# Kernel optimization log

Measured on AMD Instinct MI355X. Metric: run time of the kernel, lower is better.

Reference implementation:

```python
import jax, jax.numpy as jnp
import numpy as np
import math

HIDDEN = 1024
HEADS = 16
HEAD_DIM = HIDDEN // HEADS
B, S = 2, 2048


def setup_inputs() -> dict:
    key = jax.random.key(0)
    ks = jax.random.split(key, 10)
    std = 1.0 / math.sqrt(HIDDEN)
    mk = lambda k: (jax.random.normal(k, (HIDDEN, HIDDEN), jnp.float32) * std)
    return {
        "hidden_states": jax.random.normal(ks[0], (B, S, HIDDEN), jnp.float32),
        "attention_mask": jnp.zeros((B, 1, 1, S), jnp.float32),
        "wq": mk(ks[1]), "bq": jnp.zeros((HIDDEN,), jnp.float32),
        "wk": mk(ks[2]), "bk": jnp.zeros((HIDDEN,), jnp.float32),
        "wv": mk(ks[3]), "bv": jnp.zeros((HIDDEN,), jnp.float32),
        "wo": mk(ks[4]), "bo": jnp.zeros((HIDDEN,), jnp.float32),
    }


def reference(hidden_states, attention_mask, wq, bq, wk, bk, wv, bv, wo, bo):
    b, s, _ = hidden_states.shape
    scale = math.sqrt(HEAD_DIM)
    # projections (torch Linear: x @ W.T + b); weights stored as [out, in]
    q = hidden_states @ wq.T + bq
    k = hidden_states @ wk.T + bk
    v = hidden_states @ wv.T + bv
    # [B, H, S, D]
    q = q.reshape(b, s, HEADS, HEAD_DIM).transpose(0, 2, 1, 3)
    k = k.reshape(b, s, HEADS, HEAD_DIM).transpose(0, 2, 1, 3)
    v = v.reshape(b, s, HEADS, HEAD_DIM).transpose(0, 2, 1, 3)
    scores = jnp.einsum("bhqd,bhkd->bhqk", q, k) / scale
    scores = scores + attention_mask  # broadcast [B,1,1,S]
    weights = jax.nn.softmax(scores, axis=-1)  # dropout = identity (eval)
    out = jnp.einsum("bhqk,bhkd->bhqd", weights, v)
    out = out.transpose(0, 2, 1, 3).reshape(b, s, HIDDEN)
    out = out @ wo.T + bo
    return out
```

## Files before the change

### kernel.cpp

```cpp
#include <hip/hip_runtime.h>
#include <hip/hip_bf16.h>

typedef __bf16 bf16_t;
typedef __bf16 bf16x8 __attribute__((ext_vector_type(8)));
typedef _Float16 f16x4 __attribute__((ext_vector_type(4)));
typedef _Float16 f16x8 __attribute__((ext_vector_type(8)));
typedef float f32x4 __attribute__((ext_vector_type(4)));

#define SEQ    2048
#define NH     16
#define HD     64
#define HIDDEN 1024
#define LOG2E  1.44269504f

#if __has_builtin(__builtin_amdgcn_exp2f)
#define EXP2F(x) __builtin_amdgcn_exp2f(x)
#else
#define EXP2F(x) exp2f(x)
#endif

__device__ __forceinline__ bf16_t to_bf16(float f) { return (bf16_t)f; }

__device__ __forceinline__ void async16(const void* g, void* l) {
    __builtin_amdgcn_global_load_lds((const __attribute__((address_space(1))) void*)g,
                                     (__attribute__((address_space(3))) void*)l, 16, 0, 0);
}

__global__ __launch_bounds__(256) void cvt_kernel(
    const float* __restrict__ s0, bf16_t* __restrict__ d0, int c0,
    const float* __restrict__ s1, bf16_t* __restrict__ d1, int c1,
    const float* __restrict__ s2, bf16_t* __restrict__ d2, int c2,
    const float* __restrict__ s3, bf16_t* __restrict__ d3, int c3,
    const float* __restrict__ s4, bf16_t* __restrict__ d4, int c4,
    const float* __restrict__ s5, float* __restrict__ d5)
{
    int blk = blockIdx.x;
    const float* s; bf16_t* d;
    if (blk < c0)              { s = s0; d = d0; }
    else if ((blk -= c0) < c1) { s = s1; d = d1; }
    else if ((blk -= c1) < c2) { s = s2; d = d2; }
    else if ((blk -= c2) < c3) { s = s3; d = d3; }
    else if ((blk -= c3) < c4) { s = s4; d = d4; }
    else {
        blk -= c4;
        const size_t base = (size_t)blk * 2048 + threadIdx.x * 8;
        float4 a = *(const float4*)&s5[base];
        float4 b = *(const float4*)&s5[base + 4];
        a.x *= LOG2E; a.y *= LOG2E; a.z *= LOG2E; a.w *= LOG2E;
        b.x *= LOG2E; b.y *= LOG2E; b.z *= LOG2E; b.w *= LOG2E;
        *(float4*)&d5[base] = a;
        *(float4*)&d5[base + 4] = b;
        return;
    }
    const size_t base = (size_t)blk * 2048 + threadIdx.x * 8;
    const float4 a = *(const float4*)&s[base];
    const float4 b = *(const float4*)&s[base + 4];
    bf16x8 o;
    o[0] = (bf16_t)a.x; o[1] = (bf16_t)a.y; o[2] = (bf16_t)a.z; o[3] = (bf16_t)a.w;
    o[4] = (bf16_t)b.x; o[5] = (bf16_t)b.y; o[6] = (bf16_t)b.z; o[7] = (bf16_t)b.w;
    *(bf16x8*)&d[base] = o;
}

__global__ __launch_bounds__(256, 3) void qkv_kernel(
    const bf16_t* __restrict__ X,
    const bf16_t* __restrict__ wq, const bf16_t* __restrict__ wk, const bf16_t* __restrict__ wv,
    const float* __restrict__ bq, const float* __restrict__ bk, const float* __restrict__ bv,
    bf16_t* __restrict__ qws, bf16_t* __restrict__ kws, _Float16* __restrict__ vws)
{
    __shared__ __align__(16) bf16_t Sh[16384];
    const int z = blockIdx.z;
    const bf16_t* Wsel = (z == 0) ? wq : (z == 1) ? wk : wv;
    const float*  bsel = (z == 0) ? bq : (z == 1) ? bk : bv;
    const int m0 = blockIdx.y * 128, n0 = blockIdx.x * 128;

    const int t = threadIdx.x, lane = t & 63, w = t >> 6;
    const int w0 = w & 1, w1 = w >> 1, l15 = lane & 15, q4 = lane >> 4;

    f32x4 acc[4][4];
#pragma unroll
    for (int i = 0; i < 4; i++)
#pragma unroll
        for (int j = 0; j < 4; j++) acc[i][j] = f32x4{0.f, 0.f, 0.f, 0.f};

    auto stage = [&](int kt, int buf) {
#pragma unroll
        for (int j = 0; j < 2; j++) {
            const int s = j * 256 + t;
            const int row = s >> 2, c = (s & 3) ^ (row & 3);
            const int lb = buf * 8192 + (j * 256 + w * 64) * 8;
            async16(&X[(size_t)(m0 + row) * HIDDEN + kt + c * 8], &Sh[lb]);
            async16(&Wsel[(size_t)(n0 + row) * HIDDEN + kt + c * 8], &Sh[lb + 4096]);
        }
    };
    stage(0, 0);

    for (int it = 0; it < 32; it++) {
        const int cur = it & 1;
        __syncthreads();
        if (it < 31) stage((it + 1) * 32, cur ^ 1);
        const bf16_t* As = &Sh[cur * 8192];
        const bf16_t* Bs = &Sh[cur * 8192 + 4096];
        bf16x8 af[4];
#pragma unroll
        for (int ti = 0; ti < 4; ti++) {
            const int ra = w0 * 64 + ti * 16 + l15;
            af[ti] = *(const bf16x8*)&As[ra * 32 + (q4 ^ (ra & 3)) * 8];
        }
#pragma unroll
        for (int tj = 0; tj < 4; tj++) {
            const int rb = w1 * 64 + tj * 16 + l15;
            const bf16x8 bfr = *(const bf16x8*)&Bs[rb * 32 + (q4 ^ (rb & 3)) * 8];
#pragma unroll
            for (int ti = 0; ti < 4; ti++)
                acc[ti][tj] = __builtin_amdgcn_mfma_f32_16x16x32_bf16(af[ti], bfr, acc[ti][tj], 0, 0, 0);
        }
    }
    __syncthreads();

    if (z < 2) {
#pragma unroll
        for (int tj = 0; tj < 4; tj++) {
            const int n = w1 * 64 + tj * 16 + l15;
            const float bb = bsel[n0 + n];
            const int ch = (n >> 3), sub = n & 7;
#pragma unroll
            for (int ti = 0; ti < 4; ti++)
#pragma unroll
                for (int r = 0; r < 4; r++) {
                    const int m = w0 * 64 + ti * 16 + q4 * 4 + r;
                    Sh[m * 128 + ((ch ^ (m & 15)) << 3) + sub] = to_bf16(acc[ti][tj][r] + bb);
                }
        }
        __syncthreads();
        bf16_t* dst = (z == 0) ? qws : kws;
#pragma unroll
        for (int i = 0; i < 8; i++) {
            const int g = i * 256 + t;
            const int row = g >> 4, c = g & 15;
            const bf16x8 vv = *(const bf16x8*)&Sh[row * 128 + ((c ^ (row & 15)) << 3)];
            *(bf16x8*)&dst[(size_t)(m0 + row) * HIDDEN + n0 + c * 8] = vv;
        }
    } else {
        _Float16* Vt = (_Float16*)Sh;
#pragma unroll
        for (int tj = 0; tj < 4; tj++) {
            const int n = w1 * 64 + tj * 16 + l15;
            const float bb = bsel[n0 + n];
#pragma unroll
            for (int ti = 0; ti < 4; ti++) {
                const int mb = w0 * 64 + ti * 16 + q4 * 4;
                f16x4 v;
#pragma unroll
                for (int r = 0; r < 4; r++) v[r] = (_Float16)(acc[ti][tj][r] + bb);
                *(f16x4*)&Vt[n * 128 + (((mb >> 3) ^ (n & 15)) << 3) + (mb & 7)] = v;
            }
        }
        __syncthreads();
        const int b = m0 >> 11, sbase = m0 & (SEQ - 1);
#pragma unroll
        for (int i = 0; i < 8; i++) {
            const int g = i * 256 + t;
            const int row = g >> 4, c = g & 15;
            const int sA = (c >> 2) * 32 + (c & 3) * 4;
            const int sB = sA + 16;
            const f16x4 va = *(const f16x4*)&Vt[row * 128 + (((sA >> 3) ^ (row & 15)) << 3) + (sA & 7)];
            const f16x4 vb = *(const f16x4*)&Vt[row * 128 + (((sB >> 3) ^ (row & 15)) << 3) + (sB & 7)];
            f16x8 vv;
            vv[0] = va[0]; vv[1] = va[1]; vv[2] = va[2]; vv[3] = va[3];
            vv[4] = vb[0]; vv[5] = vb[1]; vv[6] = vb[2]; vv[7] = vb[3];
            const int d = (n0 + row) & 63, hh = (n0 + row) >> 6;
            *(f16x8*)&vws[(((size_t)b * NH + hh) * HD + d) * SEQ + sbase + c * 8] = vv;
        }
    }
}

__global__ __launch_bounds__(256, 4) void attn_kernel(
    const bf16_t* __restrict__ Qw, const bf16_t* __restrict__ Kw,
    const _Float16* __restrict__ Vtw, const float* __restrict__ Msc,
    bf16_t* __restrict__ Ow)
{
    __shared__ __align__(16) bf16_t Tiles[2][2][64 * 64];

    const int t = threadIdx.x, lane = t & 63, w = t >> 6;
    const int l15 = lane & 15, q4 = lane >> 4;
    const int lid = blockIdx.x;
    const int c8 = lid & 7, jx = lid >> 3;
    const int bh = c8 * 4 + (jx >> 5);
    const int q0 = (jx & 31) * 64;
    const int b = bh >> 4, h = bh & 15;

    const bf16_t* Qh = Qw + (size_t)b * SEQ * HIDDEN + h * HD;
    const bf16_t* Kh = Kw + (size_t)b * SEQ * HIDDEN + h * HD;
    const _Float16* Vh = Vtw + (size_t)bh * HD * SEQ;
    const float* Mrow = Msc + (size_t)b * SEQ;

    const int qrow = q0 + w * 16 + l15;
    bf16x8 qf[2];
#pragma unroll
    for (int ks = 0; ks < 2; ks++)
        qf[ks] = *(const bf16x8*)&Qh[(size_t)qrow * HIDDEN + ks * 32 + q4 * 8];

    f32x4 oacc[4];
#pragma unroll
    for (int nb = 0; nb < 4; nb++) oacc[nb] = f32x4{0.f, 0.f, 0.f, 0.f};
    float psum = 0.f;

    int koff[8];
#pragma unroll
    for (int cb = 0; cb < 4; cb++)
#pragma unroll
        for (int ks = 0; ks < 2; ks++) {
            const int rk = cb * 16 + l15;
            koff[cb * 2 + ks] = rk * 64 + (((ks * 4 + q4) ^ (rk & 7)) << 3);
        }
    int voff[8];
#pragma unroll
    for (int t2 = 0; t2 < 2; t2++)
#pragma unroll
        for (int nb = 0; nb < 4; nb++) {
            const int rv = nb * 16 + l15;
            voff[t2 * 4 + nb] = rv * 64 + (((t2 * 4 + q4) ^ (rv & 7)) << 3);
        }

    const int rs0 = t >> 3, cs0 = (t & 7) ^ (rs0 & 7);
    const int rs1 = 32 + rs0, cs1 = (t & 7) ^ (rs1 & 7);
    const bf16_t*   Kp0 = Kh + (size_t)rs0 * HIDDEN + cs0 * 8;
    const bf16_t*   Kp1 = Kh + (size_t)rs1 * HIDDEN + cs1 * 8;
    const _Float16* Vp0 = Vh + (size_t)rs0 * SEQ + cs0 * 8;
    const _Float16* Vp1 = Vh + (size_t)rs1 * SEQ + cs1 * 8;
    const int db0 = (0 * 256 + w * 64) * 8, db1 = (1 * 256 + w * 64) * 8;

    auto stageKV = [&](int it, int buf) {
        const int kt = it * 64;
        bf16_t*   Kd = &Tiles[buf][0][0];
        _Float16* Vd = (_Float16*)&Tiles[buf][1][0];
        async16(Kp0 + (size_t)kt * HIDDEN, &Kd[db0]);
        async16(Vp0 + kt,                  &Vd[db0]);
        async16(Kp1 + (size_t)kt * HIDDEN, &Kd[db1]);
        async16(Vp1 + kt,                  &Vd[db1]);
    };

    auto iterBody = [&](int it, int buf) {
        __syncthreads();
        if (it < 31) stageKV(it + 1, buf ^ 1);

        const bf16_t*   Ksh = &Tiles[buf][0][0];
        const _Float16* Vsh = (const _Float16*)&Tiles[buf][1][0];

        float4 mv4[4];
#pragma unroll
        for (int cb = 0; cb < 4; cb++) mv4[cb] = *(const float4*)&Mrow[it * 64 + cb * 16 + q4 * 4];

        f32x4 sa[4];
#pragma unroll
        for (int cb = 0; cb < 4; cb++) sa[cb] = f32x4{0.f, 0.f, 0.f, 0.f};
#pragma unroll
        for (int cb = 0; cb < 4; cb++)
#pragma unroll
            for (int ks = 0; ks < 2; ks++) {
                const bf16x8 kf = *(const bf16x8*)&Ksh[koff[cb * 2 + ks]];
                sa[cb] = __builtin_amdgcn_mfma_f32_16x16x32_bf16(kf, qf[ks], sa[cb], 0, 0, 0);
            }

        f16x8 pa[2];
#pragma unroll
        for (int cb = 0; cb < 4; cb++) {
            const float4 mv = mv4[cb];
            const float mk[4] = {mv.x, mv.y, mv.z, mv.w};
            float p[4];
#pragma unroll
            for (int r = 0; r < 4; r++) {
                p[r] = EXP2F(fmaf(sa[cb][r], 0.125f * LOG2E, mk[r]));
                pa[cb >> 1][(cb & 1) * 4 + r] = (_Float16)p[r];
            }
            psum += (p[0] + p[1]) + (p[2] + p[3]);
        }

#pragma unroll
        for (int t2 = 0; t2 < 2; t2++)
#pragma unroll
            for (int nb = 0; nb < 4; nb++) {
                const f16x8 vf = *(const f16x8*)&Vsh[voff[t2 * 4 + nb]];
                oacc[nb] = __builtin_amdgcn_mfma_f32_16x16x32_f16(pa[t2], vf, oacc[nb], 0, 0, 0);
            }
    };

    stageKV(0, 0);
#pragma unroll 1
    for (int it2 = 0; it2 < 16; it2++) {
        iterBody(it2 * 2, 0);
        iterBody(it2 * 2 + 1, 1);
    }

    psum += __shfl_xor(psum, 16);
    psum += __shfl_xor(psum, 32);

    float inv[4];
#pragma unroll
    for (int r = 0; r < 4; r++) inv[r] = 1.f / __shfl(psum, q4 * 4 + r);
#pragma unroll
    for (int r = 0; r < 4; r++) {
        const int srow = q0 + w * 16 + q4 * 4 + r;
#pragma unroll
        for (int nb = 0; nb < 4; nb++)
            Ow[((size_t)b * SEQ + srow) * HIDDEN + h * HD + nb * 16 + l15] =
                to_bf16(oacc[nb][r] * inv[r]);
    }
}

__global__ __launch_bounds__(256, 2) void oproj_kernel(
    const bf16_t* __restrict__ A, const bf16_t* __restrict__ Wo,
    const float* __restrict__ bo, float* __restrict__ Out)
{
    __shared__ __align__(16) bf16_t Sh[12288];
    const int m0 = blockIdx.y * 64, n0 = blockIdx.x * 128;
    const int t = threadIdx.x, lane = t & 63, w = t >> 6;
    const int l15 = lane & 15, q4 = lane >> 4;

    f32x4 acc[4][2];
#pragma unroll
    for (int i = 0; i < 4; i++)
#pragma unroll
        for (int j = 0; j < 2; j++) acc[i][j] = f32x4{0.f, 0.f, 0.f, 0.f};

    auto stage = [&](int kt, int buf) {
        {
            const int row = t >> 2, c = (t & 3) ^ (row & 3);
            async16(&A[(size_t)(m0 + row) * HIDDEN + kt + c * 8], &Sh[buf * 6144 + w * 64 * 8]);
        }
#pragma unroll
        for (int j = 0; j < 2; j++) {
            const int s = j * 256 + t;
            const int row = s >> 2, c = (s & 3) ^ (row & 3);
            async16(&Wo[(size_t)(n0 + row) * HIDDEN + kt + c * 8],
                    &Sh[buf * 6144 + 2048 + (j * 256 + w * 64) * 8]);
        }
    };
    stage(0, 0);

    for (int it = 0; it < 32; it++) {
        const int cur = it & 1;
        __syncthreads();
        if (it < 31) stage((it + 1) * 32, cur ^ 1);
        const bf16_t* As = &Sh[cur * 6144];
        const bf16_t* Bs = &Sh[cur * 6144 + 2048];
        bf16x8 af[4];
#pragma unroll
        for (int ti = 0; ti < 4; ti++) {
            const int ra = ti * 16 + l15;
            af[ti] = *(const bf16x8*)&As[ra * 32 + (q4 ^ (ra & 3)) * 8];
        }
#pragma unroll
        for (int tj = 0; tj < 2; tj++) {
            const int rb = w * 32 + tj * 16 + l15;
            const bf16x8 bfr = *(const bf16x8*)&Bs[rb * 32 + (q4 ^ (rb & 3)) * 8];
#pragma unroll
            for (int ti = 0; ti < 4; ti++)
                acc[ti][tj] = __builtin_amdgcn_mfma_f32_16x16x32_bf16(bfr, af[ti], acc[ti][tj], 0, 0, 0);
        }
    }

#pragma unroll
    for (int tj = 0; tj < 2; tj++) {
        const int nb4 = n0 + w * 32 + tj * 16 + q4 * 4;
        const float4 bb = *(const float4*)&bo[nb4];
#pragma unroll
        for (int ti = 0; ti < 4; ti++) {
            const int m = m0 + ti * 16 + l15;
            float4 ov;
            ov.x = acc[ti][tj][0] + bb.x;
            ov.y = acc[ti][tj][1] + bb.y;
            ov.z = acc[ti][tj][2] + bb.z;
            ov.w = acc[ti][tj][3] + bb.w;
            *(float4*)&Out[(size_t)m * HIDDEN + nb4] = ov;
        }
    }
}

extern "C" void kernel_launch(void* const* d_in, const int* in_sizes, int n_in,
                              void* d_out, int out_size, void* d_ws, size_t ws_size,
                              hipStream_t stream) {
    const float* X   = (const float*)d_in[0];
    const float* msk = (const float*)d_in[1];
    const float* wq  = (const float*)d_in[2];
    const float* bq  = (const float*)d_in[3];
    const float* wk  = (const float*)d_in[4];
    const float* bk  = (const float*)d_in[5];
    const float* wv  = (const float*)d_in[6];
    const float* bv  = (const float*)d_in[7];
    const float* wo  = (const float*)d_in[8];
    const float* bo  = (const float*)d_in[9];
    float* out = (float*)d_out;

    const size_t NELT = (size_t)2 * SEQ * HIDDEN;
    const size_t WELT = (size_t)HIDDEN * HIDDEN;
    bf16_t*    xbf = (bf16_t*)d_ws;
    bf16_t*    qws = xbf + NELT;
    bf16_t*    kws = qws + NELT;
    _Float16*  vws = (_Float16*)(kws + NELT);
    bf16_t*    aws = xbf;
    bf16_t*    wqb = (bf16_t*)d_out;
    bf16_t*    wkb = wqb + WELT;
    bf16_t*    wvb = wkb + WELT;
    bf16_t*    wob = wvb + WELT;
    float*     mws = (float*)(wob + WELT);

    cvt_kernel<<<dim3(2048 + 4 * 512 + 2), dim3(256), 0, stream>>>(
        X, xbf, 2048, wq, wqb, 512, wk, wkb, 512, wv, wvb, 512, wo, wob, 512,
        msk, mws);
    qkv_kernel<<<dim3(8, 32, 3), dim3(256), 0, stream>>>(
        xbf, wqb, wkb, wvb, bq, bk, bv, qws, kws, vws);
    attn_kernel<<<dim3(1024), dim3(256), 0, stream>>>(qws, kws, vws, mws, aws);
    oproj_kernel<<<dim3(8, 64), dim3(256), 0, stream>>>(aws, wob, bo, out);
}
```

Measured before the change: 192.8 us.

## Process two query tiles per wave to reuse K/V tiles, compute rowsum via MFMA

Each attention block now handles 128 query rows, with every wave computing two 16-row query tiles against the same K/V shared-memory tiles. This halves the grid and the K/V load traffic per query row. The softmax denominator is now accumulated with an MFMA against a ones vector instead of scalar adds and cross-lane shuffles. Register pressure rises, so the launch bound drops to 2 blocks per SM, which lowers occupancy.

```diff
diff --git a/kernel.cpp b/kernel.cpp
--- a/kernel.cpp
+++ b/kernel.cpp
@@ -174,7 +174,7 @@
     }
 }
 
-__global__ __launch_bounds__(256, 4) void attn_kernel(
+__global__ __launch_bounds__(256, 2) void attn_kernel(
     const bf16_t* __restrict__ Qw, const bf16_t* __restrict__ Kw,
     const _Float16* __restrict__ Vtw, const float* __restrict__ Msc,
     bf16_t* __restrict__ Ow)
@@ -185,8 +185,8 @@
     const int l15 = lane & 15, q4 = lane >> 4;
     const int lid = blockIdx.x;
     const int c8 = lid & 7, jx = lid >> 3;
-    const int bh = c8 * 4 + (jx >> 5);
-    const int q0 = (jx & 31) * 64;
+    const int bh = c8 * 4 + (jx >> 4);
+    const int q0 = (jx & 15) * 128;
     const int b = bh >> 4, h = bh & 15;
 
     const bf16_t* Qh = Qw + (size_t)b * SEQ * HIDDEN + h * HD;
@@ -194,16 +194,25 @@
     const _Float16* Vh = Vtw + (size_t)bh * HD * SEQ;
     const float* Mrow = Msc + (size_t)b * SEQ;
 
-    const int qrow = q0 + w * 16 + l15;
-    bf16x8 qf[2];
-#pragma unroll
-    for (int ks = 0; ks < 2; ks++)
-        qf[ks] = *(const bf16x8*)&Qh[(size_t)qrow * HIDDEN + ks * 32 + q4 * 8];
-
-    f32x4 oacc[4];
-#pragma unroll
-    for (int nb = 0; nb < 4; nb++) oacc[nb] = f32x4{0.f, 0.f, 0.f, 0.f};
-    float psum = 0.f;
+    bf16x8 qf[2][2];
+#pragma unroll
+    for (int nq = 0; nq < 2; nq++)
+#pragma unroll
+        for (int ks = 0; ks < 2; ks++)
+            qf[nq][ks] = *(const bf16x8*)&Qh[(size_t)(q0 + w * 32 + nq * 16 + l15) * HIDDEN + ks * 32 + q4 * 8];
+
+    f32x4 oacc[2][4];
+#pragma unroll
+    for (int nq = 0; nq < 2; nq++)
+#pragma unroll
+        for (int nb = 0; nb < 4; nb++) oacc[nq][nb] = f32x4{0.f, 0.f, 0.f, 0.f};
+    f32x4 osum[2];
+    osum[0] = f32x4{0.f, 0.f, 0.f, 0.f};
+    osum[1] = f32x4{0.f, 0.f, 0.f, 0.f};
+
+    f16x8 vone;
+#pragma unroll
+    for (int i = 0; i < 8; i++) vone[i] = (_Float16)1.0f;
 
     int koff[8];
 #pragma unroll
@@ -251,29 +260,32 @@
 #pragma unroll
         for (int cb = 0; cb < 4; cb++) mv4[cb] = *(const float4*)&Mrow[it * 64 + cb * 16 + q4 * 4];
 
-        f32x4 sa[4];
-#pragma unroll
-        for (int cb = 0; cb < 4; cb++) sa[cb] = f32x4{0.f, 0.f, 0.f, 0.f};
+        f32x4 sa[2][4];
+#pragma unroll
+        for (int nq = 0; nq < 2; nq++)
+#pragma unroll
+            for (int cb = 0; cb < 4; cb++) sa[nq][cb] = f32x4{0.f, 0.f, 0.f, 0.f};
 #pragma unroll
         for (int cb = 0; cb < 4; cb++)
 #pragma unroll
             for (int ks = 0; ks < 2; ks++) {
                 const bf16x8 kf = *(const bf16x8*)&Ksh[koff[cb * 2 + ks]];
-                sa[cb] = __builtin_amdgcn_mfma_f32_16x16x32_bf16(kf, qf[ks], sa[cb], 0, 0, 0);
+                sa[0][cb] = __builtin_amdgcn_mfma_f32_16x16x32_bf16(kf, qf[0][ks], sa[0][cb], 0, 0, 0);
+                sa[1][cb] = __builtin_amdgcn_mfma_f32_16x16x32_bf16(kf, qf[1][ks], sa[1][cb], 0, 0, 0);
             }
 
-        f16x8 pa[2];
+        f16x8 pa[2][2];
 #pragma unroll
         for (int cb = 0; cb < 4; cb++) {
             const float4 mv = mv4[cb];
             const float mk[4] = {mv.x, mv.y, mv.z, mv.w};
-            float p[4];
-#pragma unroll
-            for (int r = 0; r < 4; r++) {
-                p[r] = EXP2F(fmaf(sa[cb][r], 0.125f * LOG2E, mk[r]));
-                pa[cb >> 1][(cb & 1) * 4 + r] = (_Float16)p[r];
-            }
-            psum += (p[0] + p[1]) + (p[2] + p[3]);
+#pragma unroll
+            for (int nq = 0; nq < 2; nq++)
+#pragma unroll
+                for (int r = 0; r < 4; r++) {
+                    const float p = EXP2F(fmaf(sa[nq][cb][r], 0.125f * LOG2E, mk[r]));
+                    pa[nq][cb >> 1][(cb & 1) * 4 + r] = (_Float16)p;
+                }
         }
 
 #pragma unroll
@@ -281,8 +293,15 @@
 #pragma unroll
             for (int nb = 0; nb < 4; nb++) {
                 const f16x8 vf = *(const f16x8*)&Vsh[voff[t2 * 4 + nb]];
-                oacc[nb] = __builtin_amdgcn_mfma_f32_16x16x32_f16(pa[t2], vf, oacc[nb], 0, 0, 0);
+                oacc[0][nb] = __builtin_amdgcn_mfma_f32_16x16x32_f16(pa[0][t2], vf, oacc[0][nb], 0, 0, 0);
+                oacc[1][nb] = __builtin_amdgcn_mfma_f32_16x16x32_f16(pa[1][t2], vf, oacc[1][nb], 0, 0, 0);
             }
+
+#pragma unroll
+        for (int nq = 0; nq < 2; nq++)
+#pragma unroll
+            for (int t2 = 0; t2 < 2; t2++)
+                osum[nq] = __builtin_amdgcn_mfma_f32_16x16x32_f16(pa[nq][t2], vone, osum[nq], 0, 0, 0);
     };
 
     stageKV(0, 0);
@@ -292,19 +311,19 @@
         iterBody(it2 * 2 + 1, 1);
     }
 
-    psum += __shfl_xor(psum, 16);
-    psum += __shfl_xor(psum, 32);
-
-    float inv[4];
-#pragma unroll
-    for (int r = 0; r < 4; r++) inv[r] = 1.f / __shfl(psum, q4 * 4 + r);
-#pragma unroll
-    for (int r = 0; r < 4; r++) {
-        const int srow = q0 + w * 16 + q4 * 4 + r;
-#pragma unroll
-        for (int nb = 0; nb < 4; nb++)
-            Ow[((size_t)b * SEQ + srow) * HIDDEN + h * HD + nb * 16 + l15] =
-                to_bf16(oacc[nb][r] * inv[r]);
+#pragma unroll
+    for (int nq = 0; nq < 2; nq++) {
+        float inv[4];
+#pragma unroll
+        for (int r = 0; r < 4; r++) inv[r] = 1.f / osum[nq][r];
+#pragma unroll
+        for (int r = 0; r < 4; r++) {
+            const int srow = q0 + w * 32 + nq * 16 + q4 * 4 + r;
+#pragma unroll
+            for (int nb = 0; nb < 4; nb++)
+                Ow[((size_t)b * SEQ + srow) * HIDDEN + h * HD + nb * 16 + l15] =
+                    to_bf16(oacc[nq][nb][r] * inv[r]);
+        }
     }
 }
 
@@ -410,6 +429,6 @@
         msk, mws);
     qkv_kernel<<<dim3(8, 32, 3), dim3(256), 0, stream>>>(
         xbf, wqb, wkb, wvb, bq, bk, bv, qws, kws, vws);
-    attn_kernel<<<dim3(1024), dim3(256), 0, stream>>>(qws, kws, vws, mws, aws);
+    attn_kernel<<<dim3(512), dim3(256), 0, stream>>>(qws, kws, vws, mws, aws);
     oproj_kernel<<<dim3(8, 64), dim3(256), 0, stream>>>(aws, wob, bo, out);
 }
```

Result: no change. 194.9 us (+1.1%).
